# Performance work log

Measured on AMD Instinct MI355X. Metric: run time of the kernel, lower is better.

Reference implementation:

```python
import jax, jax.numpy as jnp
import numpy as np

H, DH = 8, 64          # heads, dim_head
INNER = H * DH         # 512
LN_EPS = 1e-5


def setup_inputs() -> dict:
    key = jax.random.key(0)
    ks = jax.random.split(key, 6)
    Q, NW, D = 8192, 5, 640
    return {
        "q": jax.random.normal(ks[0], (Q, NW, D), jnp.float32),
        "k": jax.random.normal(ks[1], (Q, 1, D), jnp.float32),
        "v": jax.random.normal(ks[2], (Q, 1, D), jnp.float32),
        "ln_g": jnp.ones((D,), jnp.float32),
        "ln_b": jnp.zeros((D,), jnp.float32),
        "W_in": jax.random.normal(ks[3], (D, INNER), jnp.float32) * (D ** -0.5),
        "W_out": jax.random.normal(ks[4], (INNER, D), jnp.float32) * (INNER ** -0.5),
        "b_out": jnp.zeros((D,), jnp.float32),
        "variance_scale": jnp.ones((1,), jnp.float32),
        "covariance_scale": jnp.ones((1,), jnp.float32),
    }


def _proj(x, g, b, W):
    # LayerNorm (biased var, eps=1e-5) + Linear(no bias), then 'q n (h d) -> h q n d'
    mu = x.mean(-1, keepdims=True)
    var = x.var(-1, keepdims=True)
    xn = (x - mu) * jax.lax.rsqrt(var + LN_EPS) * g + b
    y = xn @ W  # (Q, N, INNER)
    Qd, N, _ = y.shape
    return y.reshape(Qd, N, H, DH).transpose(2, 0, 1, 3)  # (h, Q, N, d)


def reference(q, k, v, ln_g, ln_b, W_in, W_out, b_out, variance_scale, covariance_scale):
    f_q = _proj(q, ln_g, ln_b, W_in)  # (h, Q, n_way, d)
    f_k = _proj(k, ln_g, ln_b, W_in)  # (h, Q, 1, d)
    f_v = _proj(v, ln_g, ln_b, W_in)  # (h, Q, 1, d)

    # cosine distance: dots / outer(||q||, ||k||)
    dots = jnp.matmul(f_q, jnp.swapaxes(f_k, -1, -2))        # (h, Q, n_way, 1)
    nq = jnp.linalg.norm(f_q, axis=-1)                        # (h, Q, n_way)
    nk = jnp.linalg.norm(f_k, axis=-1)                        # (h, Q, 1)
    dots = dots / jnp.einsum('hqi,hqj->hqij', nq, nk)

    # variance-based weights (q1 == q2, n2 == 1 branch)
    var_q = f_q.var(-1) + 1e-6                                # (h, Q, n_way)
    var_k = f_k.var(-1) + 1e-6                                # (h, Q, 1)
    vw = 1.0 / (jnp.abs(var_k - var_q) + 1e-6)                # broadcast (h, Q, n_way)
    vw = vw / (vw.sum(-1, keepdims=True) + 1e-6)
    dots = dots + variance_scale * vw[..., None]

    # covariance-based weights (q1 == q2 branch)
    fqn = f_q - f_q.mean(-1, keepdims=True)                   # (h, Q, n_way, d)
    fkn = (f_k - f_k.mean(-1, keepdims=True))[:, :, 0, :]     # (h, Q, d)
    cov = jnp.einsum('hqd,hqnd->hqn', fkn, fqn) / (DH + 1e-6)
    dots = dots + covariance_scale * jax.nn.sigmoid(cov)[..., None]

    # NOTE: cosine variant applies NO softmax (faithful to original)
    out = jnp.matmul(dots, f_v)                               # (h, Q, n_way, d)
    h, Qd, N, d = out.shape
    out = out.transpose(1, 2, 0, 3).reshape(Qd, N, h * d)     # 'h q n d -> q n (h d)'
    return out @ W_out + b_out
```

## Files before the change

### kernel.cpp

```cpp
#include <hip/hip_runtime.h>
#include <hip/hip_bf16.h>

typedef __bf16 bf16_t;
typedef __bf16 bf16x8 __attribute__((ext_vector_type(8)));
typedef float  f32x4  __attribute__((ext_vector_type(4)));

#define DEV __device__ __forceinline__

static constexpr int QN    = 8192;
static constexpr int NW    = 5;
static constexpr int D     = 640;
static constexpr int INNER = 512;
static constexpr int MQ    = QN * NW;

DEV float wredsum(float x) {
#pragma unroll
  for (int o = 32; o > 0; o >>= 1) x += __shfl_xor(x, o, 64);
  return x;
}

DEV void gl_lds16(const bf16_t* g, bf16_t* l) {
  __builtin_amdgcn_global_load_lds(
      (const __attribute__((address_space(1))) unsigned int*)g,
      (__attribute__((address_space(3))) unsigned int*)l, 16, 0, 0);
}

__global__ __launch_bounds__(256) void ln_split_kernel(
    const float* __restrict__ q, const float* __restrict__ k,
    const float* __restrict__ v, const float* __restrict__ g,
    const float* __restrict__ b, bf16_t* __restrict__ Ah,
    bf16_t* __restrict__ Al, int row0) {
  int lr   = blockIdx.x * 4 + (threadIdx.x >> 6);
  int lane = threadIdx.x & 63;
  int rg   = row0 + lr;
  const float* src = (rg < MQ) ? q + (size_t)rg * D
                   : (rg < MQ + QN) ? k + (size_t)(rg - MQ) * D
                   : v + (size_t)(rg - MQ - QN) * D;
  float2 x[5];
  float s = 0.f, ss = 0.f;
#pragma unroll
  for (int j = 0; j < 5; ++j) {
    x[j] = ((const float2*)src)[lane + 64 * j];
    s  += x[j].x + x[j].y;
    ss += x[j].x * x[j].x + x[j].y * x[j].y;
  }
  s = wredsum(s); ss = wredsum(ss);
  float m  = s * (1.f / D);
  float rs = rsqrtf(ss * (1.f / D) - m * m + 1e-5f);
#pragma unroll
  for (int j = 0; j < 5; ++j) {
    float2 gg = ((const float2*)g)[lane + 64 * j];
    float2 bb = ((const float2*)b)[lane + 64 * j];
    float xn0 = (x[j].x - m) * rs * gg.x + bb.x;
    float xn1 = (x[j].y - m) * rs * gg.y + bb.y;
    bf16_t h0 = (bf16_t)xn0, h1 = (bf16_t)xn1;
    union { bf16_t bb2[2]; unsigned u; } ph, pl;
    ph.bb2[0] = h0; ph.bb2[1] = h1;
    pl.bb2[0] = (bf16_t)(xn0 - (float)h0);
    pl.bb2[1] = (bf16_t)(xn1 - (float)h1);
    ((unsigned*)(Ah + (size_t)lr * D))[lane + 64 * j] = ph.u;
    ((unsigned*)(Al + (size_t)lr * D))[lane + 64 * j] = pl.u;
  }
}

__global__ void transpose_split_kernel(const float* __restrict__ src,
                                       bf16_t* __restrict__ dstH,
                                       bf16_t* __restrict__ dstL, int R, int C) {
  int idx = blockIdx.x * 256 + threadIdx.x;
  if (idx >= R * C) return;
  int r = idx / C, c = idx - r * C;
  float x  = src[idx];
  bf16_t h = (bf16_t)x;
  dstH[(size_t)c * R + r] = h;
  dstL[(size_t)c * R + r] = (bf16_t)(x - (float)h);
}

template <int MODE>
__global__ __launch_bounds__(256) void gemm1_kernel(
    const bf16_t* __restrict__ Ah, const bf16_t* __restrict__ Al,
    const bf16_t* __restrict__ Bh, const bf16_t* __restrict__ Bl,
    float* __restrict__ Fkv, const float* __restrict__ Fk,
    float* __restrict__ Sq, float* __restrict__ Sqq,
    float* __restrict__ Sqk, int qrow0) {
  __shared__ __align__(16) bf16_t AhS[128 * 32];
  __shared__ __align__(16) bf16_t AlS[128 * 32];
  __shared__ __align__(16) bf16_t BhS[128 * 32];
  __shared__ __align__(16) bf16_t BlS[128 * 32];
  const unsigned wg = (blockIdx.x & 7) * (gridDim.x >> 3) + (blockIdx.x >> 3);
  const int bn = wg & 3, bm = wg >> 2;
  const int t = threadIdx.x, lane = t & 63, wid = t >> 6;
  const int wr = wid >> 1, wc = wid & 1;
  const int lm = lane & 15, quad = lane >> 4;
  const bool T3 = (MODE == 1) || (bm < 64);
  const size_t arow0 = (size_t)bm * 128;
  const size_t brow0 = (size_t)bn * 128;
  const int cb = wid * 2;
  const int sx = (lm >> 1) & 3;

  auto STAGE = [&](int k0) {
#pragma unroll
    for (int tt = 0; tt < 2; ++tt) {
      int chunk = (cb + tt) * 64 + lane;
      int r = chunk >> 2;
      int c8 = (((chunk & 3) ^ ((r >> 1) & 3)) * 8);
      gl_lds16(Ah + (arow0 + r) * 640 + k0 + c8, &AhS[(cb + tt) * 512]);
      gl_lds16(Bh + (brow0 + r) * 640 + k0 + c8, &BhS[(cb + tt) * 512]);
      if (T3) {
        gl_lds16(Al + (arow0 + r) * 640 + k0 + c8, &AlS[(cb + tt) * 512]);
        gl_lds16(Bl + (brow0 + r) * 640 + k0 + c8, &BlS[(cb + tt) * 512]);
      }
    }
  };

  f32x4 acc[4][4] = {};
  STAGE(0);

  for (int k0 = 0; k0 < 640; k0 += 32) {
    __syncthreads();
    bf16x8 ah[4], bh[4], al[4], bl[4];
#pragma unroll
    for (int i = 0; i < 4; ++i) {
      ah[i] = *(const bf16x8*)&AhS[(wr * 64 + i * 16 + lm) * 32 + (quad ^ sx) * 8];
      bh[i] = *(const bf16x8*)&BhS[(wc * 64 + i * 16 + lm) * 32 + (quad ^ sx) * 8];
    }
    if (T3) {
#pragma unroll
      for (int i = 0; i < 4; ++i) {
        al[i] = *(const bf16x8*)&AlS[(wr * 64 + i * 16 + lm) * 32 + (quad ^ sx) * 8];
        bl[i] = *(const bf16x8*)&BlS[(wc * 64 + i * 16 + lm) * 32 + (quad ^ sx) * 8];
      }
    }
    __syncthreads();
    if (k0 + 32 < 640) STAGE(k0 + 32);
#pragma unroll
    for (int mi = 0; mi < 4; ++mi)
#pragma unroll
      for (int nj = 0; nj < 4; ++nj) {
        acc[mi][nj] =
            __builtin_amdgcn_mfma_f32_16x16x32_bf16(ah[mi], bh[nj], acc[mi][nj], 0, 0, 0);
        if (T3) {
          acc[mi][nj] =
              __builtin_amdgcn_mfma_f32_16x16x32_bf16(al[mi], bh[nj], acc[mi][nj], 0, 0, 0);
          acc[mi][nj] =
              __builtin_amdgcn_mfma_f32_16x16x32_bf16(ah[mi], bl[nj], acc[mi][nj], 0, 0, 0);
        }
      }
  }

  if (MODE == 0) {
#pragma unroll
    for (int mi = 0; mi < 4; ++mi)
#pragma unroll
      for (int nj = 0; nj < 4; ++nj)
#pragma unroll
        for (int r = 0; r < 4; ++r) {
          int row = bm * 128 + wr * 64 + mi * 16 + quad * 4 + r;
          int col = bn * 128 + wc * 64 + nj * 16 + lm;
          Fkv[(size_t)row * INNER + col] = acc[mi][nj][r];
        }
  } else {
    const int head = bn * 2 + wc;
#pragma unroll
    for (int mi = 0; mi < 4; ++mi)
#pragma unroll
      for (int r = 0; r < 4; ++r) {
        int rowA = qrow0 + bm * 128 + wr * 64 + mi * 16 + quad * 4 + r;
        int qi   = (unsigned)rowA / NW;
        float s1 = 0.f, s2 = 0.f, s3 = 0.f;
#pragma unroll
        for (int nj = 0; nj < 4; ++nj) {
          float fq = acc[mi][nj][r];
          float fk = Fk[(size_t)qi * INNER + head * 64 + nj * 16 + lm];
          s1 += fq; s2 += fq * fq; s3 += fq * fk;
        }
#pragma unroll
        for (int o = 1; o < 16; o <<= 1) {
          s1 += __shfl_xor(s1, o, 64);
          s2 += __shfl_xor(s2, o, 64);
          s3 += __shfl_xor(s3, o, 64);
        }
        if (lm == 0) {
          size_t o = (size_t)rowA * 8 + head;
          Sq[o] = s1; Sqq[o] = s2; Sqk[o] = s3;
        }
      }
  }
}

__global__ __launch_bounds__(256) void dots_y_kernel(
    const float* __restrict__ Fkv, const float* __restrict__ Sq,
    const float* __restrict__ Sqq, const float* __restrict__ Sqk,
    const float* __restrict__ vsp, const float* __restrict__ csp,
    bf16_t* __restrict__ Yh) {
  int wv   = blockIdx.x * 4 + (threadIdx.x >> 6);
  int lane = threadIdx.x & 63;
  int qi = wv >> 3, h = wv & 7;
  float fk = Fkv[(size_t)qi * INNER + h * 64 + lane];
  float fv = Fkv[(size_t)(QN + qi) * INNER + h * 64 + lane];
  float sk  = wredsum(fk);
  float skk = wredsum(fk * fk);
  float mk   = sk * (1.f / 64.f);
  float vark = skk * (1.f / 64.f) - mk * mk + 1e-6f;
  float nk   = sqrtf(skk);

  int n = (lane < NW) ? lane : 0;
  size_t si = (size_t)(qi * NW + n) * 8 + h;
  float s1 = Sq[si], s2 = Sqq[si], s3 = Sqk[si];
  float mq   = s1 * (1.f / 64.f);
  float varq = s2 * (1.f / 64.f) - mq * mq + 1e-6f;
  float nq   = sqrtf(s2);
  float cosv = s3 / (nq * nk);
  float vw   = 1.f / (fabsf(vark - varq) + 1e-6f);
  float cov  = (s3 - 64.f * mk * mq) / (64.f + 1e-6f);
  float sg   = 1.f / (1.f + expf(-cov));
  float vwsum = 0.f;
#pragma unroll
  for (int j = 0; j < NW; ++j) vwsum += __shfl(vw, j, 64);
  float dv = cosv + vsp[0] * vw / (vwsum + 1e-6f) + csp[0] * sg;
#pragma unroll
  for (int j = 0; j < NW; ++j) {
    float dvj = __shfl(dv, j, 64);
    Yh[(size_t)(qi * NW + j) * INNER + h * 64 + lane] = (bf16_t)(dvj * fv);
  }
}

__global__ __launch_bounds__(256) void gemm2_kernel(
    const bf16_t* __restrict__ Yh, const bf16_t* __restrict__ Bh,
    const float* __restrict__ bias, float* __restrict__ out) {
  __shared__ __align__(16) bf16_t AS[128 * 32];
  __shared__ __align__(16) bf16_t BS[128 * 32];
  const unsigned wg = (blockIdx.x & 7) * (gridDim.x >> 3) + (blockIdx.x >> 3);
  const int bn = wg % 5, bm = wg / 5;
  const int t = threadIdx.x, lane = t & 63, wid = t >> 6;
  const int wr = wid >> 1, wc = wid & 1;
  const int lm = lane & 15, quad = lane >> 4;
  const size_t arow0 = (size_t)bm * 128;
  const size_t brow0 = (size_t)bn * 128;
  const int cb = wid * 2;
  const int sx = (lm >> 1) & 3;

  auto STAGE = [&](int k0) {
#pragma unroll
    for (int tt = 0; tt < 2; ++tt) {
      int chunk = (cb + tt) * 64 + lane;
      int r = chunk >> 2;
      int c8 = (((chunk & 3) ^ ((r >> 1) & 3)) * 8);
      gl_lds16(Yh + (arow0 + r) * INNER + k0 + c8, &AS[(cb + tt) * 512]);
      gl_lds16(Bh + (brow0 + r) * INNER + k0 + c8, &BS[(cb + tt) * 512]);
    }
  };

  f32x4 acc[4][4] = {};
  STAGE(0);

  for (int k0 = 0; k0 < INNER; k0 += 32) {
    __syncthreads();
    bf16x8 a[4], b[4];
#pragma unroll
    for (int i = 0; i < 4; ++i) {
      a[i] = *(const bf16x8*)&AS[(wr * 64 + i * 16 + lm) * 32 + (quad ^ sx) * 8];
      b[i] = *(const bf16x8*)&BS[(wc * 64 + i * 16 + lm) * 32 + (quad ^ sx) * 8];
    }
    __syncthreads();
    if (k0 + 32 < INNER) STAGE(k0 + 32);
#pragma unroll
    for (int mi = 0; mi < 4; ++mi)
#pragma unroll
      for (int nj = 0; nj < 4; ++nj)
        acc[mi][nj] =
            __builtin_amdgcn_mfma_f32_16x16x32_bf16(a[mi], b[nj], acc[mi][nj], 0, 0, 0);
  }
#pragma unroll
  for (int mi = 0; mi < 4; ++mi)
#pragma unroll
    for (int nj = 0; nj < 4; ++nj) {
      float bia = bias[bn * 128 + wc * 64 + nj * 16 + lm];
#pragma unroll
      for (int r = 0; r < 4; ++r) {
        int row = bm * 128 + wr * 64 + mi * 16 + quad * 4 + r;
        int col = bn * 128 + wc * 64 + nj * 16 + lm;
        out[(size_t)row * D + col] = acc[mi][nj][r] + bia;
      }
    }
}

extern "C" void kernel_launch(void* const* d_in, const int* in_sizes, int n_in,
                              void* d_out, int out_size, void* d_ws,
                              size_t ws_size, hipStream_t stream) {
  const float* q    = (const float*)d_in[0];
  const float* k    = (const float*)d_in[1];
  const float* v    = (const float*)d_in[2];
  const float* g    = (const float*)d_in[3];
  const float* b    = (const float*)d_in[4];
  const float* Win  = (const float*)d_in[5];
  const float* Wout = (const float*)d_in[6];
  const float* bout = (const float*)d_in[7];
  const float* vsp  = (const float*)d_in[8];
  const float* csp  = (const float*)d_in[9];
  float* out = (float*)d_out;

  char* w = (char*)d_ws;
  float* Fkv     = (float*)w;  w += (size_t)(2 * QN) * INNER * 4;
  float* Sq      = (float*)w;  w += (size_t)MQ * 8 * 4;
  float* Sqq     = (float*)w;  w += (size_t)MQ * 8 * 4;
  float* Sqk     = (float*)w;  w += (size_t)MQ * 8 * 4;
  bf16_t* Ah     = (bf16_t*)w; w += (size_t)MQ * D * 2;
  bf16_t* Al     = (bf16_t*)w; w += (size_t)MQ * D * 2;
  bf16_t* WinTh  = (bf16_t*)w; w += (size_t)INNER * D * 2;
  bf16_t* WinTl  = (bf16_t*)w; w += (size_t)INNER * D * 2;
  bf16_t* WoutTh = (bf16_t*)w; w += (size_t)D * INNER * 2;
  bf16_t* WoutTl = (bf16_t*)w; w += (size_t)D * INNER * 2;
  bf16_t* Yh = Ah;

  transpose_split_kernel<<<dim3((D * INNER + 255) / 256), dim3(256), 0, stream>>>(
      Win, WinTh, WinTl, D, INNER);
  transpose_split_kernel<<<dim3((INNER * D + 255) / 256), dim3(256), 0, stream>>>(
      Wout, WoutTh, WoutTl, INNER, D);

  ln_split_kernel<<<dim3(2 * QN / 4), dim3(256), 0, stream>>>(
      q, k, v, g, b, Ah, Al, MQ);
  gemm1_kernel<0><<<dim3((2 * QN / 128) * 4), dim3(256), 0, stream>>>(
      Ah, Al, WinTh, WinTl, Fkv, nullptr, nullptr, nullptr, nullptr, 0);

  ln_split_kernel<<<dim3(MQ / 4), dim3(256), 0, stream>>>(
      q, k, v, g, b, Ah, Al, 0);
  gemm1_kernel<1><<<dim3((MQ / 128) * 4), dim3(256), 0, stream>>>(
      Ah, Al, WinTh, WinTl, nullptr, Fkv, Sq, Sqq, Sqk, 0);

  dots_y_kernel<<<dim3(QN * 8 / 4), dim3(256), 0, stream>>>(
      Fkv, Sq, Sqq, Sqk, vsp, csp, Yh);
  gemm2_kernel<<<dim3((MQ / 128) * 5), dim3(256), 0, stream>>>(
      Yh, WoutTh, bout, out);
}
```

Before: 430.8 us.

## Double-buffer LDS in GEMM kernels, tile weight transpose, interleave MODE0 rows

```diff
diff --git a/kernel.cpp b/kernel.cpp
--- a/kernel.cpp
+++ b/kernel.cpp
@@ -63,16 +63,32 @@
   }
 }
 
-__global__ void transpose_split_kernel(const float* __restrict__ src,
-                                       bf16_t* __restrict__ dstH,
-                                       bf16_t* __restrict__ dstL, int R, int C) {
-  int idx = blockIdx.x * 256 + threadIdx.x;
-  if (idx >= R * C) return;
-  int r = idx / C, c = idx - r * C;
-  float x  = src[idx];
-  bf16_t h = (bf16_t)x;
-  dstH[(size_t)c * R + r] = h;
-  dstL[(size_t)c * R + r] = (bf16_t)(x - (float)h);
+__global__ __launch_bounds__(256) void transpose_split_kernel(
+    const float* __restrict__ src, bf16_t* __restrict__ dstH,
+    bf16_t* __restrict__ dstL, int R, int C) {
+  __shared__ unsigned T[64][65];
+  int tiles_c = C >> 6;
+  int tr = blockIdx.x / tiles_c, tc = blockIdx.x - tr * tiles_c;
+  int r0 = tr << 6, c0 = tc << 6;
+  int lane = threadIdx.x & 63, wid = threadIdx.x >> 6;
+#pragma unroll
+  for (int i = 0; i < 16; ++i) {
+    int r = wid * 16 + i;
+    float x = src[(size_t)(r0 + r) * C + c0 + lane];
+    bf16_t h = (bf16_t)x;
+    union { bf16_t b2[2]; unsigned u; } p;
+    p.b2[0] = h; p.b2[1] = (bf16_t)(x - (float)h);
+    T[r][lane] = p.u;
+  }
+  __syncthreads();
+#pragma unroll
+  for (int i = 0; i < 16; ++i) {
+    int c = wid * 16 + i;
+    union { bf16_t b2[2]; unsigned u; } p;
+    p.u = T[lane][c];
+    dstH[(size_t)(c0 + c) * R + r0 + lane] = p.b2[0];
+    dstL[(size_t)(c0 + c) * R + r0 + lane] = p.b2[1];
+  }
 }
 
 template <int MODE>
@@ -82,12 +98,14 @@
     float* __restrict__ Fkv, const float* __restrict__ Fk,
     float* __restrict__ Sq, float* __restrict__ Sqq,
     float* __restrict__ Sqk, int qrow0) {
-  __shared__ __align__(16) bf16_t AhS[128 * 32];
-  __shared__ __align__(16) bf16_t AlS[128 * 32];
-  __shared__ __align__(16) bf16_t BhS[128 * 32];
-  __shared__ __align__(16) bf16_t BlS[128 * 32];
+  __shared__ __align__(16) bf16_t AhS[2][128 * 32];
+  __shared__ __align__(16) bf16_t AlS[2][128 * 32];
+  __shared__ __align__(16) bf16_t BhS[2][128 * 32];
+  __shared__ __align__(16) bf16_t BlS[2][128 * 32];
   const unsigned wg = (blockIdx.x & 7) * (gridDim.x >> 3) + (blockIdx.x >> 3);
-  const int bn = wg & 3, bm = wg >> 2;
+  const int bn = wg & 3;
+  const int bm0 = wg >> 2;
+  const int bm = (MODE == 0) ? ((bm0 & 1) ? 64 + (bm0 >> 1) : (bm0 >> 1)) : bm0;
   const int t = threadIdx.x, lane = t & 63, wid = t >> 6;
   const int wr = wid >> 1, wc = wid & 1;
   const int lm = lane & 15, quad = lane >> 4;
@@ -97,41 +115,42 @@
   const int cb = wid * 2;
   const int sx = (lm >> 1) & 3;
 
-  auto STAGE = [&](int k0) {
+  auto STAGE = [&](int k0, int buf) {
 #pragma unroll
     for (int tt = 0; tt < 2; ++tt) {
       int chunk = (cb + tt) * 64 + lane;
       int r = chunk >> 2;
       int c8 = (((chunk & 3) ^ ((r >> 1) & 3)) * 8);
-      gl_lds16(Ah + (arow0 + r) * 640 + k0 + c8, &AhS[(cb + tt) * 512]);
-      gl_lds16(Bh + (brow0 + r) * 640 + k0 + c8, &BhS[(cb + tt) * 512]);
+      gl_lds16(Ah + (arow0 + r) * 640 + k0 + c8, &AhS[buf][(cb + tt) * 512]);
+      gl_lds16(Bh + (brow0 + r) * 640 + k0 + c8, &BhS[buf][(cb + tt) * 512]);
       if (T3) {
-        gl_lds16(Al + (arow0 + r) * 640 + k0 + c8, &AlS[(cb + tt) * 512]);
-        gl_lds16(Bl + (brow0 + r) * 640 + k0 + c8, &BlS[(cb + tt) * 512]);
+        gl_lds16(Al + (arow0 + r) * 640 + k0 + c8, &AlS[buf][(cb + tt) * 512]);
+        gl_lds16(Bl + (brow0 + r) * 640 + k0 + c8, &BlS[buf][(cb + tt) * 512]);
       }
     }
   };
 
   f32x4 acc[4][4] = {};
-  STAGE(0);
+  STAGE(0, 0);
+  __syncthreads();
 
   for (int k0 = 0; k0 < 640; k0 += 32) {
-    __syncthreads();
+    const int cur = (k0 >> 5) & 1;
+    if (k0 + 32 < 640) STAGE(k0 + 32, cur ^ 1);
     bf16x8 ah[4], bh[4], al[4], bl[4];
 #pragma unroll
     for (int i = 0; i < 4; ++i) {
-      ah[i] = *(const bf16x8*)&AhS[(wr * 64 + i * 16 + lm) * 32 + (quad ^ sx) * 8];
-      bh[i] = *(const bf16x8*)&BhS[(wc * 64 + i * 16 + lm) * 32 + (quad ^ sx) * 8];
+      ah[i] = *(const bf16x8*)&AhS[cur][(wr * 64 + i * 16 + lm) * 32 + (quad ^ sx) * 8];
+      bh[i] = *(const bf16x8*)&BhS[cur][(wc * 64 + i * 16 + lm) * 32 + (quad ^ sx) * 8];
     }
     if (T3) {
 #pragma unroll
       for (int i = 0; i < 4; ++i) {
-        al[i] = *(const bf16x8*)&AlS[(wr * 64 + i * 16 + lm) * 32 + (quad ^ sx) * 8];
-        bl[i] = *(const bf16x8*)&BlS[(wc * 64 + i * 16 + lm) * 32 + (quad ^ sx) * 8];
-      }
-    }
-    __syncthreads();
-    if (k0 + 32 < 640) STAGE(k0 + 32);
+        al[i] = *(const bf16x8*)&AlS[cur][(wr * 64 + i * 16 + lm) * 32 + (quad ^ sx) * 8];
+        bl[i] = *(const bf16x8*)&BlS[cur][(wc * 64 + i * 16 + lm) * 32 + (quad ^ sx) * 8];
+      }
+    }
+    __builtin_amdgcn_s_setprio(1);
 #pragma unroll
     for (int mi = 0; mi < 4; ++mi)
 #pragma unroll
@@ -145,6 +164,8 @@
               __builtin_amdgcn_mfma_f32_16x16x32_bf16(ah[mi], bl[nj], acc[mi][nj], 0, 0, 0);
         }
       }
+    __builtin_amdgcn_s_setprio(0);
+    __syncthreads();
   }
 
   if (MODE == 0) {
@@ -227,8 +248,8 @@
 __global__ __launch_bounds__(256) void gemm2_kernel(
     const bf16_t* __restrict__ Yh, const bf16_t* __restrict__ Bh,
     const float* __restrict__ bias, float* __restrict__ out) {
-  __shared__ __align__(16) bf16_t AS[128 * 32];
-  __shared__ __align__(16) bf16_t BS[128 * 32];
+  __shared__ __align__(16) bf16_t AS[2][128 * 32];
+  __shared__ __align__(16) bf16_t BS[2][128 * 32];
   const unsigned wg = (blockIdx.x & 7) * (gridDim.x >> 3) + (blockIdx.x >> 3);
   const int bn = wg % 5, bm = wg / 5;
   const int t = threadIdx.x, lane = t & 63, wid = t >> 6;
@@ -239,36 +260,39 @@
   const int cb = wid * 2;
   const int sx = (lm >> 1) & 3;
 
-  auto STAGE = [&](int k0) {
+  auto STAGE = [&](int k0, int buf) {
 #pragma unroll
     for (int tt = 0; tt < 2; ++tt) {
       int chunk = (cb + tt) * 64 + lane;
       int r = chunk >> 2;
       int c8 = (((chunk & 3) ^ ((r >> 1) & 3)) * 8);
-      gl_lds16(Yh + (arow0 + r) * INNER + k0 + c8, &AS[(cb + tt) * 512]);
-      gl_lds16(Bh + (brow0 + r) * INNER + k0 + c8, &BS[(cb + tt) * 512]);
+      gl_lds16(Yh + (arow0 + r) * INNER + k0 + c8, &AS[buf][(cb + tt) * 512]);
+      gl_lds16(Bh + (brow0 + r) * INNER + k0 + c8, &BS[buf][(cb + tt) * 512]);
     }
   };
 
   f32x4 acc[4][4] = {};
-  STAGE(0);
+  STAGE(0, 0);
+  __syncthreads();
 
   for (int k0 = 0; k0 < INNER; k0 += 32) {
-    __syncthreads();
+    const int cur = (k0 >> 5) & 1;
+    if (k0 + 32 < INNER) STAGE(k0 + 32, cur ^ 1);
     bf16x8 a[4], b[4];
 #pragma unroll
     for (int i = 0; i < 4; ++i) {
-      a[i] = *(const bf16x8*)&AS[(wr * 64 + i * 16 + lm) * 32 + (quad ^ sx) * 8];
-      b[i] = *(const bf16x8*)&BS[(wc * 64 + i * 16 + lm) * 32 + (quad ^ sx) * 8];
-    }
-    __syncthreads();
-    if (k0 + 32 < INNER) STAGE(k0 + 32);
+      a[i] = *(const bf16x8*)&AS[cur][(wr * 64 + i * 16 + lm) * 32 + (quad ^ sx) * 8];
+      b[i] = *(const bf16x8*)&BS[cur][(wc * 64 + i * 16 + lm) * 32 + (quad ^ sx) * 8];
+    }
+    __builtin_amdgcn_s_setprio(1);
 #pragma unroll
     for (int mi = 0; mi < 4; ++mi)
 #pragma unroll
       for (int nj = 0; nj < 4; ++nj)
         acc[mi][nj] =
             __builtin_amdgcn_mfma_f32_16x16x32_bf16(a[mi], b[nj], acc[mi][nj], 0, 0, 0);
+    __builtin_amdgcn_s_setprio(0);
+    __syncthreads();
   }
 #pragma unroll
   for (int mi = 0; mi < 4; ++mi)
@@ -312,9 +336,9 @@
   bf16_t* WoutTl = (bf16_t*)w; w += (size_t)D * INNER * 2;
   bf16_t* Yh = Ah;
 
-  transpose_split_kernel<<<dim3((D * INNER + 255) / 256), dim3(256), 0, stream>>>(
+  transpose_split_kernel<<<dim3((D / 64) * (INNER / 64)), dim3(256), 0, stream>>>(
       Win, WinTh, WinTl, D, INNER);
-  transpose_split_kernel<<<dim3((INNER * D + 255) / 256), dim3(256), 0, stream>>>(
+  transpose_split_kernel<<<dim3((INNER / 64) * (D / 64)), dim3(256), 0, stream>>>(
       Wout, WoutTh, WoutTl, INNER, D);
 
   ln_split_kernel<<<dim3(2 * QN / 4), dim3(256), 0, stream>>>(
```

New measurement: 432.9 us. Within noise of the previous version (+0.5%).

## Fuse Y construction into gemm2 A-tile staging, tile weight transpose, remap gemm1 rows

Applied to the files above, without the earlier changes.

```diff
diff --git a/kernel.cpp b/kernel.cpp
--- a/kernel.cpp
+++ b/kernel.cpp
@@ -63,16 +63,32 @@
   }
 }
 
-__global__ void transpose_split_kernel(const float* __restrict__ src,
-                                       bf16_t* __restrict__ dstH,
-                                       bf16_t* __restrict__ dstL, int R, int C) {
-  int idx = blockIdx.x * 256 + threadIdx.x;
-  if (idx >= R * C) return;
-  int r = idx / C, c = idx - r * C;
-  float x  = src[idx];
-  bf16_t h = (bf16_t)x;
-  dstH[(size_t)c * R + r] = h;
-  dstL[(size_t)c * R + r] = (bf16_t)(x - (float)h);
+__global__ __launch_bounds__(256) void transpose_split_kernel(
+    const float* __restrict__ src, bf16_t* __restrict__ dstH,
+    bf16_t* __restrict__ dstL, int R, int C) {
+  __shared__ unsigned T[64][65];
+  int tiles_c = C >> 6;
+  int tr = blockIdx.x / tiles_c, tc = blockIdx.x - tr * tiles_c;
+  int r0 = tr << 6, c0 = tc << 6;
+  int lane = threadIdx.x & 63, wid = threadIdx.x >> 6;
+#pragma unroll
+  for (int i = 0; i < 16; ++i) {
+    int r = wid * 16 + i;
+    float x = src[(size_t)(r0 + r) * C + c0 + lane];
+    bf16_t h = (bf16_t)x;
+    union { bf16_t b2[2]; unsigned u; } p;
+    p.b2[0] = h; p.b2[1] = (bf16_t)(x - (float)h);
+    T[r][lane] = p.u;
+  }
+  __syncthreads();
+#pragma unroll
+  for (int i = 0; i < 16; ++i) {
+    int c = wid * 16 + i;
+    union { bf16_t b2[2]; unsigned u; } p;
+    p.u = T[lane][c];
+    dstH[(size_t)(c0 + c) * R + r0 + lane] = p.b2[0];
+    dstL[(size_t)(c0 + c) * R + r0 + lane] = p.b2[1];
+  }
 }
 
 template <int MODE>
@@ -87,7 +103,9 @@
   __shared__ __align__(16) bf16_t BhS[128 * 32];
   __shared__ __align__(16) bf16_t BlS[128 * 32];
   const unsigned wg = (blockIdx.x & 7) * (gridDim.x >> 3) + (blockIdx.x >> 3);
-  const int bn = wg & 3, bm = wg >> 2;
+  const int bn = wg & 3;
+  const int bm0 = wg >> 2;
+  const int bm = (MODE == 0) ? ((bm0 & 1) ? 64 + (bm0 >> 1) : (bm0 >> 1)) : bm0;
   const int t = threadIdx.x, lane = t & 63, wid = t >> 6;
   const int wr = wid >> 1, wc = wid & 1;
   const int lm = lane & 15, quad = lane >> 4;
@@ -187,16 +205,15 @@
   }
 }
 
-__global__ __launch_bounds__(256) void dots_y_kernel(
+__global__ __launch_bounds__(256) void dots_kernel(
     const float* __restrict__ Fkv, const float* __restrict__ Sq,
     const float* __restrict__ Sqq, const float* __restrict__ Sqk,
     const float* __restrict__ vsp, const float* __restrict__ csp,
-    bf16_t* __restrict__ Yh) {
+    float* __restrict__ Dv) {
   int wv   = blockIdx.x * 4 + (threadIdx.x >> 6);
   int lane = threadIdx.x & 63;
   int qi = wv >> 3, h = wv & 7;
   float fk = Fkv[(size_t)qi * INNER + h * 64 + lane];
-  float fv = Fkv[(size_t)(QN + qi) * INNER + h * 64 + lane];
   float sk  = wredsum(fk);
   float skk = wredsum(fk * fk);
   float mk   = sk * (1.f / 64.f);
@@ -217,16 +234,13 @@
 #pragma unroll
   for (int j = 0; j < NW; ++j) vwsum += __shfl(vw, j, 64);
   float dv = cosv + vsp[0] * vw / (vwsum + 1e-6f) + csp[0] * sg;
-#pragma unroll
-  for (int j = 0; j < NW; ++j) {
-    float dvj = __shfl(dv, j, 64);
-    Yh[(size_t)(qi * NW + j) * INNER + h * 64 + lane] = (bf16_t)(dvj * fv);
-  }
+  if (lane < NW) Dv[(size_t)(qi * NW + lane) * 8 + h] = dv;
 }
 
 __global__ __launch_bounds__(256) void gemm2_kernel(
-    const bf16_t* __restrict__ Yh, const bf16_t* __restrict__ Bh,
-    const float* __restrict__ bias, float* __restrict__ out) {
+    const float* __restrict__ Fkv, const float* __restrict__ Dv,
+    const bf16_t* __restrict__ Bh, const float* __restrict__ bias,
+    float* __restrict__ out) {
   __shared__ __align__(16) bf16_t AS[128 * 32];
   __shared__ __align__(16) bf16_t BS[128 * 32];
   const unsigned wg = (blockIdx.x & 7) * (gridDim.x >> 3) + (blockIdx.x >> 3);
@@ -234,27 +248,60 @@
   const int t = threadIdx.x, lane = t & 63, wid = t >> 6;
   const int wr = wid >> 1, wc = wid & 1;
   const int lm = lane & 15, quad = lane >> 4;
-  const size_t arow0 = (size_t)bm * 128;
   const size_t brow0 = (size_t)bn * 128;
   const int cb = wid * 2;
   const int sx = (lm >> 1) & 3;
 
-  auto STAGE = [&](int k0) {
+  const int r0    = t >> 1;
+  const int row_g = bm * 128 + r0;
+  const int qi    = (unsigned)row_g / NW;
+  const float* fvrow = Fkv + (size_t)(QN + qi) * INNER;
+  const float* dvrow = Dv + (size_t)row_g * 8;
+  const int aslot[2] = { ((t * 2) & 3) ^ ((r0 >> 1) & 3),
+                         ((t * 2 + 1) & 3) ^ ((r0 >> 1) & 3) };
+  const int acol[2]  = { ((t * 2) & 3) * 8, ((t * 2 + 1) & 3) * 8 };
+
+  auto STAGE_B = [&](int k0) {
 #pragma unroll
     for (int tt = 0; tt < 2; ++tt) {
       int chunk = (cb + tt) * 64 + lane;
       int r = chunk >> 2;
       int c8 = (((chunk & 3) ^ ((r >> 1) & 3)) * 8);
-      gl_lds16(Yh + (arow0 + r) * INNER + k0 + c8, &AS[(cb + tt) * 512]);
       gl_lds16(Bh + (brow0 + r) * INNER + k0 + c8, &BS[(cb + tt) * 512]);
     }
   };
 
+  f32x4 av[2][2];
+  float dvv[2];
+  auto LOAD_A = [&](int k0) {
+#pragma unroll
+    for (int u = 0; u < 2; ++u) {
+      int col = k0 + acol[u];
+      av[u][0] = *(const f32x4*)&fvrow[col];
+      av[u][1] = *(const f32x4*)&fvrow[col + 4];
+      dvv[u]   = dvrow[col >> 6];
+    }
+  };
+  auto WRITE_A = [&]() {
+#pragma unroll
+    for (int u = 0; u < 2; ++u) {
+      bf16x8 pk;
+#pragma unroll
+      for (int e = 0; e < 4; ++e) {
+        pk[e]     = (bf16_t)(dvv[u] * av[u][0][e]);
+        pk[e + 4] = (bf16_t)(dvv[u] * av[u][1][e]);
+      }
+      *(bf16x8*)&AS[r0 * 32 + aslot[u] * 8] = pk;
+    }
+  };
+
   f32x4 acc[4][4] = {};
-  STAGE(0);
+  STAGE_B(0);
+  LOAD_A(0);
+  WRITE_A();
+  __syncthreads();
 
   for (int k0 = 0; k0 < INNER; k0 += 32) {
-    __syncthreads();
     bf16x8 a[4], b[4];
 #pragma unroll
     for (int i = 0; i < 4; ++i) {
@@ -262,13 +309,16 @@
       b[i] = *(const bf16x8*)&BS[(wc * 64 + i * 16 + lm) * 32 + (quad ^ sx) * 8];
     }
     __syncthreads();
-    if (k0 + 32 < INNER) STAGE(k0 + 32);
+    const bool more = (k0 + 32 < INNER);
+    if (more) { STAGE_B(k0 + 32); LOAD_A(k0 + 32); }
 #pragma unroll
     for (int mi = 0; mi < 4; ++mi)
 #pragma unroll
       for (int nj = 0; nj < 4; ++nj)
         acc[mi][nj] =
             __builtin_amdgcn_mfma_f32_16x16x32_bf16(a[mi], b[nj], acc[mi][nj], 0, 0, 0);
+    if (more) WRITE_A();
+    __syncthreads();
   }
 #pragma unroll
   for (int mi = 0; mi < 4; ++mi)
@@ -304,17 +354,17 @@
   float* Sq      = (float*)w;  w += (size_t)MQ * 8 * 4;
   float* Sqq     = (float*)w;  w += (size_t)MQ * 8 * 4;
   float* Sqk     = (float*)w;  w += (size_t)MQ * 8 * 4;
+  float* Dv      = (float*)w;  w += (size_t)MQ * 8 * 4;
   bf16_t* Ah     = (bf16_t*)w; w += (size_t)MQ * D * 2;
   bf16_t* Al     = (bf16_t*)w; w += (size_t)MQ * D * 2;
   bf16_t* WinTh  = (bf16_t*)w; w += (size_t)INNER * D * 2;
   bf16_t* WinTl  = (bf16_t*)w; w += (size_t)INNER * D * 2;
   bf16_t* WoutTh = (bf16_t*)w; w += (size_t)D * INNER * 2;
   bf16_t* WoutTl = (bf16_t*)w; w += (size_t)D * INNER * 2;
-  bf16_t* Yh = Ah;
-
-  transpose_split_kernel<<<dim3((D * INNER + 255) / 256), dim3(256), 0, stream>>>(
+
+  transpose_split_kernel<<<dim3((D / 64) * (INNER / 64)), dim3(256), 0, stream>>>(
       Win, WinTh, WinTl, D, INNER);
-  transpose_split_kernel<<<dim3((INNER * D + 255) / 256), dim3(256), 0, stream>>>(
+  transpose_split_kernel<<<dim3((INNER / 64) * (D / 64)), dim3(256), 0, stream>>>(
       Wout, WoutTh, WoutTl, INNER, D);
 
   ln_split_kernel<<<dim3(2 * QN / 4), dim3(256), 0, stream>>>(
@@ -327,8 +377,8 @@
   gemm1_kernel<1><<<dim3((MQ / 128) * 4), dim3(256), 0, stream>>>(
       Ah, Al, WinTh, WinTl, nullptr, Fkv, Sq, Sqq, Sqk, 0);
 
-  dots_y_kernel<<<dim3(QN * 8 / 4), dim3(256), 0, stream>>>(
-      Fkv, Sq, Sqq, Sqk, vsp, csp, Yh);
+  dots_kernel<<<dim3(QN * 8 / 4), dim3(256), 0, stream>>>(
+      Fkv, Sq, Sqq, Sqk, vsp, csp, Dv);
   gemm2_kernel<<<dim3((MQ / 128) * 5), dim3(256), 0, stream>>>(
-      Yh, WoutTh, bout, out);
-}
+      Fkv, Dv, WoutTh, bout, out);
+}
```

Measured after the change: 427.9 us. Within noise of the previous version (-0.7%).
